# Optimization experiments

Hardware: AMD Instinct MI355X
Metric: run time of the kernel (lower is better)

Reference implementation:

```python
import jax, jax.numpy as jnp
import numpy as np

EPS = 1e-5

def _bn(h, g, b, m, v):
    # h: (B, Ch, L); BatchNorm1d in eval mode over channel axis 1
    inv = jax.lax.rsqrt(v + EPS)
    return (h - m[None, :, None]) * (inv * g)[None, :, None] + b[None, :, None]

def setup_inputs() -> dict:
    key = jax.random.key(0)
    ks = jax.random.split(key, 12)
    B, C, N = 32, 256, 4096
    N8, C8 = N // 8, C // 8
    x = jax.random.normal(ks[0], (B, C, N), dtype=jnp.float32)
    Wq = jax.random.normal(ks[1], (N8, N), dtype=jnp.float32) * (1.0 / np.sqrt(N))
    Wk = jax.random.normal(ks[2], (N8, N), dtype=jnp.float32) * (1.0 / np.sqrt(N))
    bn1_g = jnp.ones((N8,), jnp.float32); bn1_b = jnp.zeros((N8,), jnp.float32)
    bn1_m = jax.random.normal(ks[3], (N8,), jnp.float32) * 0.1
    bn1_v = jax.random.uniform(ks[4], (N8,), jnp.float32, 0.5, 1.5)
    bn2_g = jnp.ones((N8,), jnp.float32); bn2_b = jnp.zeros((N8,), jnp.float32)
    bn2_m = jax.random.normal(ks[5], (N8,), jnp.float32) * 0.1
    bn2_v = jax.random.uniform(ks[6], (N8,), jnp.float32, 0.5, 1.5)
    W1 = jax.random.normal(ks[7], (C8, C), dtype=jnp.float32) * (1.0 / np.sqrt(C))
    W2 = jax.random.normal(ks[8], (C, C8), dtype=jnp.float32) * (1.0 / np.sqrt(C8))
    alpha = jax.random.normal(ks[9], (1,), dtype=jnp.float32)
    return {"x": x, "Wq": Wq, "bn1_g": bn1_g, "bn1_b": bn1_b, "bn1_m": bn1_m, "bn1_v": bn1_v,
            "Wk": Wk, "bn2_g": bn2_g, "bn2_b": bn2_b, "bn2_m": bn2_m, "bn2_v": bn2_v,
            "W1": W1, "W2": W2, "alpha": alpha}

def reference(x, Wq, bn1_g, bn1_b, bn1_m, bn1_v, Wk, bn2_g, bn2_b, bn2_m, bn2_v, W1, W2, alpha):
    # x: (B, C, N); x_hat: (B, N, C) -- conv1d with kernel 1 == matmul over N axis
    x_hat = jnp.transpose(x, (0, 2, 1))
    q = jax.nn.relu(_bn(jnp.einsum('qn,bnc->bqc', Wq, x_hat), bn1_g, bn1_b, bn1_m, bn1_v))  # (B, N8, C)
    k = jax.nn.relu(_bn(jnp.einsum('qn,bnc->bqc', Wk, x_hat), bn2_g, bn2_b, bn2_m, bn2_v))  # (B, N8, C)
    sim = jnp.einsum('bkc,bkd->bcd', k, q)  # (B, C, C)
    aff = jax.nn.softmax(jnp.max(sim, axis=-1, keepdims=True) - sim, axis=-1)
    # squeeze-excite gating over channels
    pooled = jnp.max(x, axis=-1)  # (B, C) AdaptiveMaxPool1d(1)
    s = jax.nn.sigmoid(jax.nn.relu(pooled @ W1.T) @ W2.T)  # (B, C)
    gated = x * s[:, :, None]
    out = alpha[0] * jnp.einsum('bcd,bdn->bcn', aff, gated) + x
    return out
```

## Files before the change

### kernel.cpp

```cpp
#include <hip/hip_runtime.h>
#include <math.h>

#define B_   32
#define C_   256
#define N_   4096
#define N8_  512
#define C8_  32
#define EPS_ 1e-5f

typedef __attribute__((ext_vector_type(8))) short short8;
typedef __attribute__((ext_vector_type(4))) float f32x4;

__device__ __forceinline__ ushort f2bf(float v) {
  unsigned u = __float_as_uint(v);
  unsigned r = (u + 0x7fffu + ((u >> 16) & 1u)) >> 16;
  return (ushort)r;
}
__device__ __forceinline__ float bf2f(ushort h) {
  return __uint_as_float(((unsigned)h) << 16);
}

__global__ __launch_bounds__(256) void k_cvt(const float* __restrict__ src,
                                             ushort* __restrict__ hi,
                                             ushort* __restrict__ lo, int n4) {
  int i = blockIdx.x * 256 + threadIdx.x;
  int stride = gridDim.x * 256;
  for (; i < n4; i += stride) {
    float4 v = ((const float4*)src)[i];
    ushort4 h, l;
    h.x = f2bf(v.x); l.x = f2bf(v.x - bf2f(h.x));
    h.y = f2bf(v.y); l.y = f2bf(v.y - bf2f(h.y));
    h.z = f2bf(v.z); l.z = f2bf(v.z - bf2f(h.z));
    h.w = f2bf(v.w); l.w = f2bf(v.w - bf2f(h.w));
    ((ushort4*)hi)[i] = h;
    ((ushort4*)lo)[i] = l;
  }
}

__global__ __launch_bounds__(256) void k_cvt_x(const float* __restrict__ x,
    ushort* __restrict__ xh, ushort* __restrict__ xl,
    ushort* __restrict__ xTh, float* __restrict__ partial) {
  int b = blockIdx.z, cb = blockIdx.y, nb = blockIdx.x;
  int t = threadIdx.x;
  int cl  = t >> 2;
  int nl0 = (t & 3) * 16;
  const float* xp = x + ((size_t)b * C_ + cb * 64 + cl) * N_ + nb * 64 + nl0;
  float v[16];
  *(float4*)&v[0]  = *(const float4*)(xp + 0);
  *(float4*)&v[4]  = *(const float4*)(xp + 4);
  *(float4*)&v[8]  = *(const float4*)(xp + 8);
  *(float4*)&v[12] = *(const float4*)(xp + 12);
  ushort h[16], l[16];
  float mx = -3.402823466e+38f;
  #pragma unroll
  for (int j = 0; j < 16; ++j) {
    h[j] = f2bf(v[j]);
    l[j] = f2bf(v[j] - bf2f(h[j]));
    mx = fmaxf(mx, v[j]);
  }
  size_t fbase = ((size_t)b * C_ + cb * 64 + cl) * N_ + nb * 64 + nl0;
  *(short8*)(xh + fbase)     = *(short8*)&h[0];
  *(short8*)(xh + fbase + 8) = *(short8*)&h[8];
  *(short8*)(xl + fbase)     = *(short8*)&l[0];
  *(short8*)(xl + fbase + 8) = *(short8*)&l[8];
  mx = fmaxf(mx, __shfl_xor(mx, 1, 64));
  mx = fmaxf(mx, __shfl_xor(mx, 2, 64));
  if ((t & 3) == 0)
    partial[((size_t)b * C_ + cb * 64 + cl) * 64 + nb] = mx;
  __shared__ ushort lds[64 * 66];
  #pragma unroll
  for (int j = 0; j < 16; ++j) lds[cl * 66 + nl0 + j] = h[j];
  __syncthreads();
  int nr = t >> 2;
  int c0 = (t & 3) * 16;
  ushort o[16];
  #pragma unroll
  for (int j = 0; j < 16; ++j) o[j] = lds[(c0 + j) * 66 + nr];
  size_t tbase = ((size_t)b * N_ + nb * 64 + nr) * C_ + cb * 64 + c0;
  *(short8*)(xTh + tbase)     = *(short8*)&o[0];
  *(short8*)(xTh + tbase + 8) = *(short8*)&o[8];
}

__global__ __launch_bounds__(256) void k_semlp(const float* __restrict__ partial,
                                               const float* __restrict__ W1,
                                               const float* __restrict__ W2,
                                               float* __restrict__ s) {
  int b = blockIdx.x, t = threadIdx.x;
  __shared__ float p[C_];
  __shared__ float h[C8_];
  float m = -3.402823466e+38f;
  const float* pp = partial + ((size_t)b * C_ + t) * 64;
  #pragma unroll
  for (int j = 0; j < 64; ++j) m = fmaxf(m, pp[j]);
  p[t] = m;
  __syncthreads();
  if (t < C8_) {
    float a = 0.f;
    for (int c = 0; c < C_; ++c) a = fmaf(p[c], W1[t * C_ + c], a);
    h[t] = fmaxf(a, 0.f);
  }
  __syncthreads();
  float a = 0.f;
  #pragma unroll
  for (int j = 0; j < C8_; ++j) a = fmaf(h[j], W2[t * C8_ + j], a);
  s[b * C_ + t] = 1.f / (1.f + __expf(-a));
}

#define GLD16(SRC, DSTP) __builtin_amdgcn_global_load_lds( \
    (const __attribute__((address_space(1))) void*)(SRC), \
    (__attribute__((address_space(3))) void*)(DSTP), 16, 0, 0)

__global__ __launch_bounds__(512, 2) void k_qk8(
    const ushort* __restrict__ wh, const ushort* __restrict__ wl,
    const ushort* __restrict__ xh, const ushort* __restrict__ xl,
    float* __restrict__ part) {
  __shared__ ushort lds[2][2][256 * 64];
  const int bid = blockIdx.x;
  const int xcd = bid & 7, slot = bid >> 3;
  const int b   = xcd * 4 + (slot & 3);
  const int role = slot >> 2;
  const int ks = role & 1;
  const int mt = role >> 1;
  const int t = threadIdx.x;
  const int lane = t & 63, wave = t >> 6;
  const int wm = wave >> 2, wn = wave & 3;
  const int fr = lane & 15, quad = lane >> 4;
  const int R0 = mt * 256;
  const int tr = t >> 3, tc = (t & 7) << 3;
  int aro[4], bro[4];
#pragma unroll
  for (int j = 0; j < 4; ++j) {
    int rl = j * 64 + tr;
    int cu = tc ^ ((rl & 7) << 3);
    aro[j] = (R0 + rl) * N_ + cu;
    bro[j] = (b * C_ + rl) * N_ + cu;
  }
  const int dl = t * 8;

  f32x4 acc[8][4];
#pragma unroll
  for (int m = 0; m < 8; ++m)
#pragma unroll
    for (int n = 0; n < 4; ++n) acc[m][n] = (f32x4){0.f, 0.f, 0.f, 0.f};

  short8 af[4][2];
  short8 bf[2][2][2];

#define STG_A(AP, K0, P, J0) do { \
    GLD16((AP) + (aro[J0] + (K0)), &lds[P][0][(J0) * 4096 + dl]); \
    GLD16((AP) + (aro[(J0) + 1] + (K0)), &lds[P][0][((J0) + 1) * 4096 + dl]); \
  } while (0)
#define STG_B(BP, K0, P, J0) do { \
    GLD16((BP) + (bro[J0] + (K0)), &lds[P][1][(J0) * 4096 + dl]); \
    GLD16((BP) + (bro[(J0) + 1] + (K0)), &lds[P][1][((J0) + 1) * 4096 + dl]); \
  } while (0)
#define VMC(N) asm volatile("s_waitcnt vmcnt(" #N ")" ::: "memory")
#define BARF() do { __builtin_amdgcn_s_barrier(); \
                    __builtin_amdgcn_sched_barrier(0); } while (0)
#define RDA(P, MH) do { \
    _Pragma("unroll") \
    for (int m = 0; m < 4; ++m) { \
      int r = wm * 128 + ((MH) * 4 + m) * 16 + fr; \
      int o = (r << 6); \
      int sw = (r & 7) << 3; \
      af[m][0] = *(const short8*)&lds[P][0][o + ((quad << 3) ^ sw)]; \
      af[m][1] = *(const short8*)&lds[P][0][o + (((quad << 3) + 32) ^ sw)]; \
    } } while (0)
#define RDB(P, NH) do { \
    _Pragma("unroll") \
    for (int n = 0; n < 2; ++n) { \
      int c = wn * 64 + ((NH) * 2 + n) * 16 + fr; \
      int o = (c << 6); \
      int sw = (c & 7) << 3; \
      bf[NH][n][0] = *(const short8*)&lds[P][1][o + ((quad << 3) ^ sw)]; \
      bf[NH][n][1] = *(const short8*)&lds[P][1][o + (((quad << 3) + 32) ^ sw)]; \
    } } while (0)
#define MMQ(MH, NH) do { \
    __builtin_amdgcn_s_setprio(1); \
    _Pragma("unroll") \
    for (int m = 0; m < 4; ++m) \
      _Pragma("unroll") \
      for (int n = 0; n < 2; ++n) { \
        acc[(MH)*4+m][(NH)*2+n] = __builtin_amdgcn_mfma_f32_16x16x32_bf16( \
            af[m][0], bf[NH][n][0], acc[(MH)*4+m][(NH)*2+n], 0, 0, 0); \
        acc[(MH)*4+m][(NH)*2+n] = __builtin_amdgcn_mfma_f32_16x16x32_bf16( \
            af[m][1], bf[NH][n][1], acc[(MH)*4+m][(NH)*2+n], 0, 0, 0); \
      } \
    __builtin_amdgcn_s_setprio(0); } while (0)

  const int gbase = ks * 96;
  {
    int g = gbase, sg = g >> 6, k0 = (g & 63) << 6;
    const ushort* Ap = (sg == 1) ? wl : wh;
    const ushort* Bp = (sg == 2) ? xl : xh;
    STG_A(Ap, k0, 0, 0); STG_A(Ap, k0, 0, 2);
    STG_B(Bp, k0, 0, 0); STG_B(Bp, k0, 0, 2);
    int g1 = gbase + 1, s1 = g1 >> 6, k1 = (g1 & 63) << 6;
    const ushort* Ap1 = (s1 == 1) ? wl : wh;
    STG_A(Ap1, k1, 1, 0);
  }

#pragma unroll 1
  for (int i = 0; i < 48; ++i) {
    int gO = gbase + 2 * i + 1, sO = gO >> 6, kO = (gO & 63) << 6;
    const ushort* AO = (sO == 1) ? wl : wh;
    const ushort* BO = (sO == 2) ? xl : xh;
    int gE = gbase + 2 * i + 2, sE = gE >> 6, kE = (gE & 63) << 6;
    const ushort* AE = (sE == 1) ? wl : wh;
    const ushort* BE = (sE == 2) ? xl : xh;
    int gP = gbase + 2 * i + 3, sP = gP >> 6, kP = (gP & 63) << 6;
    const ushort* APn = (sP == 1) ? wl : wh;
    const bool nl = (i < 47);
    STG_A(AO, kO, 1, 2);
    VMC(4); BARF();
    RDA(0, 0); RDB(0, 0); MMQ(0, 0);
    STG_B(BO, kO, 1, 0);
    RDB(0, 1); MMQ(0, 1);
    STG_B(BO, kO, 1, 2);
    RDA(0, 1); MMQ(1, 0);
    BARF();
    if (nl) STG_A(AE, kE, 0, 0);
    MMQ(1, 1);
    if (nl) { STG_A(AE, kE, 0, 2); VMC(4); } else { VMC(0); }
    BARF();
    RDA(1, 0); RDB(1, 0); MMQ(0, 0);
    if (nl) STG_B(BE, kE, 0, 0);
    RDB(1, 1); MMQ(0, 1);
    if (nl) STG_B(BE, kE, 0, 2);
    RDA(1, 1); MMQ(1, 0);
    BARF();
    if (nl) STG_A(APn, kP, 1, 0);
    MMQ(1, 1);
  }

  float* dst = part + ((size_t)(ks * 32 + b) * 1024) * 256;
#pragma unroll
  for (int m = 0; m < 8; ++m) {
    int row0 = R0 + wm * 128 + m * 16 + quad * 4;
#pragma unroll
    for (int r = 0; r < 4; ++r) {
#pragma unroll
      for (int n = 0; n < 4; ++n) {
        int col = wn * 64 + n * 16 + fr;
        dst[(size_t)(row0 + r) * 256 + col] = acc[m][n][r];
      }
    }
  }
#undef STG_A
#undef STG_B
#undef VMC
#undef BARF
#undef RDA
#undef RDB
#undef MMQ
}

__global__ __launch_bounds__(256) void k_qkred(
    const float* __restrict__ part,
    const float* __restrict__ g1, const float* __restrict__ b1,
    const float* __restrict__ m1, const float* __restrict__ v1,
    const float* __restrict__ g2, const float* __restrict__ b2,
    const float* __restrict__ m2, const float* __restrict__ v2,
    float* __restrict__ q, float* __restrict__ k) {
  int i = blockIdx.x * 256 + threadIdx.x;
  int b = i >> 16;
  int rem = i & 65535;
  int row = rem >> 6;
  int c4 = (rem & 63) << 2;
  const float4* p = (const float4*)part;
  float4 u = p[i];
  float4 w = p[i + 2097152];
  bool isq = row < 512;
  int m = isq ? row : row - 512;
  float sc = (isq ? g1 : g2)[m] * rsqrtf((isq ? v1 : v2)[m] + EPS_);
  float bi = (isq ? b1 : b2)[m] - (isq ? m1 : m2)[m] * sc;
  float4 o;
  o.x = fmaxf(fmaf(u.x + w.x, sc, bi), 0.f);
  o.y = fmaxf(fmaf(u.y + w.y, sc, bi), 0.f);
  o.z = fmaxf(fmaf(u.z + w.z, sc, bi), 0.f);
  o.w = fmaxf(fmaf(u.w + w.w, sc, bi), 0.f);
  float* d = (isq ? q : k) + ((size_t)b * N8_ + m) * C_ + c4;
  *(float4*)d = o;
}

__global__ __launch_bounds__(256) void k_simsoft(const float* __restrict__ q,
    const float* __restrict__ k, const float* __restrict__ s,
    const float* __restrict__ alpha, ushort* __restrict__ aff2) {
  int b = blockIdx.y, ct = blockIdx.x;
  int t = threadIdx.x;
  __shared__ float kT[N8_][16];
  const float* kb = k + (size_t)b * N8_ * C_;
  int c0 = ct * 16;
  for (int chunk = 0; chunk < N8_ / 16; ++chunk) {
    int row = chunk * 16 + (t >> 4);
    kT[row][t & 15] = kb[(size_t)row * C_ + c0 + (t & 15)];
  }
  __syncthreads();
  float acc[16];
  #pragma unroll
  for (int i = 0; i < 16; ++i) acc[i] = 0.f;
  const float* qb = q + (size_t)b * N8_ * C_;
  for (int kk = 0; kk < N8_; ++kk) {
    float qv = qb[(size_t)kk * C_ + t];
    float4 k0 = *(const float4*)&kT[kk][0];
    float4 k1 = *(const float4*)&kT[kk][4];
    float4 k2 = *(const float4*)&kT[kk][8];
    float4 k3 = *(const float4*)&kT[kk][12];
    acc[0]  = fmaf(k0.x, qv, acc[0]);  acc[1]  = fmaf(k0.y, qv, acc[1]);
    acc[2]  = fmaf(k0.z, qv, acc[2]);  acc[3]  = fmaf(k0.w, qv, acc[3]);
    acc[4]  = fmaf(k1.x, qv, acc[4]);  acc[5]  = fmaf(k1.y, qv, acc[5]);
    acc[6]  = fmaf(k1.z, qv, acc[6]);  acc[7]  = fmaf(k1.w, qv, acc[7]);
    acc[8]  = fmaf(k2.x, qv, acc[8]);  acc[9]  = fmaf(k2.y, qv, acc[9]);
    acc[10] = fmaf(k2.z, qv, acc[10]); acc[11] = fmaf(k2.w, qv, acc[11]);
    acc[12] = fmaf(k3.x, qv, acc[12]); acc[13] = fmaf(k3.y, qv, acc[13]);
    acc[14] = fmaf(k3.z, qv, acc[14]); acc[15] = fmaf(k3.w, qv, acc[15]);
  }
  int lane = t & 63, wid = t >> 6;
  __shared__ float wmin[16][4];
  __shared__ float wsum[16][4];
  #pragma unroll
  for (int i = 0; i < 16; ++i) {
    float v = acc[i];
    for (int off = 32; off > 0; off >>= 1) v = fminf(v, __shfl_xor(v, off, 64));
    if (lane == 0) wmin[i][wid] = v;
  }
  __syncthreads();
  float w[16];
  #pragma unroll
  for (int i = 0; i < 16; ++i) {
    float m = fminf(fminf(wmin[i][0], wmin[i][1]), fminf(wmin[i][2], wmin[i][3]));
    w[i] = __expf(m - acc[i]);
  }
  #pragma unroll
  for (int i = 0; i < 16; ++i) {
    float v = w[i];
    for (int off = 32; off > 0; off >>= 1) v += __shfl_xor(v, off, 64);
    if (lane == 0) wsum[i][wid] = v;
  }
  __syncthreads();
  float fac = alpha[0] * s[b * C_ + t];
  ushort* ab = aff2 + (size_t)b * C_ * C_;
  #pragma unroll
  for (int i = 0; i < 16; ++i) {
    float Z = wsum[i][0] + wsum[i][1] + wsum[i][2] + wsum[i][3];
    ab[(size_t)(c0 + i) * C_ + t] = f2bf(fac * w[i] / Z);
  }
}

__global__ __launch_bounds__(256) void k_out_mfma(
    const ushort* __restrict__ aff, const ushort* __restrict__ xTh,
    const float* __restrict__ x, float* __restrict__ out) {
  int b  = blockIdx.z;
  int cb = blockIdx.y;
  int nb = blockIdx.x;
  __shared__ ushort Ah[128 * 32];
  __shared__ ushort Bh[128 * 32];
  int t = threadIdx.x, wave = t >> 6, lane = t & 63;
  int wr = (wave >> 1) * 64, wc = (wave & 1) * 64;
  int srow = wave * 16 + (lane >> 2);
  int skof = (lane & 3) * 8;
  size_t aoff = ((size_t)b * C_ + cb * 128 + srow) * C_ + skof;
  size_t boff = ((size_t)b * N_ + nb * 128 + srow) * C_ + skof;
  int lb0 = (wave * 16) * 32;

  f32x4 acc[4][4];
  #pragma unroll
  for (int mi = 0; mi < 4; ++mi)
    #pragma unroll
    for (int ni = 0; ni < 4; ++ni)
      acc[mi][ni] = (f32x4){0.f, 0.f, 0.f, 0.f};

  int fr = lane & 15, quad = lane >> 4;
  for (int k0 = 0; k0 < C_; k0 += 32) {
    #pragma unroll
    for (int seg = 0; seg < 2; ++seg) {
      size_t ga = aoff + (size_t)seg * 64 * C_ + k0;
      size_t gb = boff + (size_t)seg * 64 * C_ + k0;
      int lb = lb0 + seg * 64 * 32;
      __builtin_amdgcn_global_load_lds(
          (const __attribute__((address_space(1))) void*)(aff + ga),
          (__attribute__((address_space(3))) void*)(&Ah[lb]), 16, 0, 0);
      __builtin_amdgcn_global_load_lds(
          (const __attribute__((address_space(1))) void*)(xTh + gb),
          (__attribute__((address_space(3))) void*)(&Bh[lb]), 16, 0, 0);
    }
    __syncthreads();
    short8 af[4], bf[4];
    #pragma unroll
    for (int i = 0; i < 4; ++i) {
      af[i] = *(const short8*)&Ah[(wr + i * 16 + fr) * 32 + quad * 8];
      bf[i] = *(const short8*)&Bh[(wc + i * 16 + fr) * 32 + quad * 8];
    }
    #pragma unroll
    for (int mi = 0; mi < 4; ++mi)
      #pragma unroll
      for (int ni = 0; ni < 4; ++ni)
        acc[mi][ni] = __builtin_amdgcn_mfma_f32_16x16x32_bf16(
            af[mi], bf[ni], acc[mi][ni], 0, 0, 0);
    __syncthreads();
  }

  const float* xb = x + (size_t)b * C_ * N_;
  float* ob = out + (size_t)b * C_ * N_;
  int c0 = cb * 128 + wr + quad * 4;
  int n0 = nb * 128 + wc + fr;
  #pragma unroll
  for (int mi = 0; mi < 4; ++mi) {
    #pragma unroll
    for (int r = 0; r < 4; ++r) {
      int c = c0 + mi * 16 + r;
      #pragma unroll
      for (int ni = 0; ni < 4; ++ni) {
        int n = n0 + ni * 16;
        ob[(size_t)c * N_ + n] = acc[mi][ni][r] + xb[(size_t)c * N_ + n];
      }
    }
  }
}

extern "C" void kernel_launch(void* const* d_in, const int* in_sizes, int n_in,
                              void* d_out, int out_size, void* d_ws, size_t ws_size,
                              hipStream_t stream) {
  const float* x     = (const float*)d_in[0];
  const float* Wq    = (const float*)d_in[1];
  const float* g1    = (const float*)d_in[2];
  const float* b1    = (const float*)d_in[3];
  const float* m1    = (const float*)d_in[4];
  const float* v1    = (const float*)d_in[5];
  const float* Wk    = (const float*)d_in[6];
  const float* g2    = (const float*)d_in[7];
  const float* b2    = (const float*)d_in[8];
  const float* m2    = (const float*)d_in[9];
  const float* v2    = (const float*)d_in[10];
  const float* W1    = (const float*)d_in[11];
  const float* W2    = (const float*)d_in[12];
  const float* alpha = (const float*)d_in[13];
  float* out = (float*)d_out;

  float* ws      = (float*)d_ws;
  float* q       = ws;
  float* kbuf    = q + (size_t)B_ * N8_ * C_;
  float* partial = kbuf + (size_t)B_ * N8_ * C_;
  float* s       = partial + (size_t)B_ * C_ * 64;
  ushort* aff    = (ushort*)(s + B_ * C_);
  ushort* xh     = aff + (size_t)B_ * C_ * C_;
  ushort* xl     = xh + (size_t)B_ * C_ * N_;
  ushort* xTh    = xl + (size_t)B_ * C_ * N_;
  ushort* wh     = xTh + (size_t)B_ * C_ * N_;
  ushort* wl     = wh + (size_t)2 * N8_ * N_;

  float* gpart = (float*)d_out;

  k_cvt_x<<<dim3(64, 4, B_), 256, 0, stream>>>(x, xh, xl, xTh, partial);
  k_cvt<<<dim3(1024), 256, 0, stream>>>(Wq, wh, wl, N8_ * N_ / 4);
  k_cvt<<<dim3(1024), 256, 0, stream>>>(Wk, wh + (size_t)N8_ * N_,
                                        wl + (size_t)N8_ * N_, N8_ * N_ / 4);
  k_semlp<<<dim3(B_), 256, 0, stream>>>(partial, W1, W2, s);
  k_qk8<<<dim3(256), 512, 0, stream>>>(wh, wl, xh, xl, gpart);
  k_qkred<<<dim3(8192), 256, 0, stream>>>(gpart, g1, b1, m1, v1,
                                          g2, b2, m2, v2, q, kbuf);
  k_simsoft<<<dim3(16, B_), 256, 0, stream>>>(q, kbuf, s, alpha, aff);
  k_out_mfma<<<dim3(32, 2, B_), 256, 0, stream>>>(aff, xTh, x, out);
}
```

Before: 648.9 us.

## Restructure QK GEMM main loop to double-buffer LDS fragments row-by-row

Rewrites the software pipeline of the split-K bf16 MFMA GEMM. Instead of staging A and B in halves interleaved with quadrant MFMA groups, each stage now issues all global-to-LDS loads at once after a barrier. LDS fragment reads are ping-ponged one A row at a time against MFMAs, and the next buffer's first fragments are prefetched before the last MFMAs finish. The aim is to hide LDS read latency and cut the number of barriers per tile, at the cost of a more complex prologue and epilogue and a different vmcnt wait discipline.

```diff
diff --git a/kernel.cpp b/kernel.cpp
--- a/kernel.cpp
+++ b/kernel.cpp
@@ -143,95 +143,107 @@
 #pragma unroll
     for (int n = 0; n < 4; ++n) acc[m][n] = (f32x4){0.f, 0.f, 0.f, 0.f};
 
-  short8 af[4][2];
-  short8 bf[2][2][2];
-
-#define STG_A(AP, K0, P, J0) do { \
-    GLD16((AP) + (aro[J0] + (K0)), &lds[P][0][(J0) * 4096 + dl]); \
-    GLD16((AP) + (aro[(J0) + 1] + (K0)), &lds[P][0][((J0) + 1) * 4096 + dl]); \
+  short8 afA_[2], afB_[2];
+  short8 b0[2][2], b1[2][2];
+
+#define STG(AP, BP, K0, P) do { \
+    GLD16((AP) + (aro[0] + (K0)), &lds[P][0][0 * 4096 + dl]); \
+    GLD16((AP) + (aro[1] + (K0)), &lds[P][0][1 * 4096 + dl]); \
+    GLD16((AP) + (aro[2] + (K0)), &lds[P][0][2 * 4096 + dl]); \
+    GLD16((AP) + (aro[3] + (K0)), &lds[P][0][3 * 4096 + dl]); \
+    GLD16((BP) + (bro[0] + (K0)), &lds[P][1][0 * 4096 + dl]); \
+    GLD16((BP) + (bro[1] + (K0)), &lds[P][1][1 * 4096 + dl]); \
+    GLD16((BP) + (bro[2] + (K0)), &lds[P][1][2 * 4096 + dl]); \
+    GLD16((BP) + (bro[3] + (K0)), &lds[P][1][3 * 4096 + dl]); \
   } while (0)
-#define STG_B(BP, K0, P, J0) do { \
-    GLD16((BP) + (bro[J0] + (K0)), &lds[P][1][(J0) * 4096 + dl]); \
-    GLD16((BP) + (bro[(J0) + 1] + (K0)), &lds[P][1][((J0) + 1) * 4096 + dl]); \
-  } while (0)
-#define VMC(N) asm volatile("s_waitcnt vmcnt(" #N ")" ::: "memory")
+#define VMC8 asm volatile("s_waitcnt vmcnt(8)" ::: "memory")
+#define VMC0 asm volatile("s_waitcnt vmcnt(0)" ::: "memory")
+#define LGKM0 asm volatile("s_waitcnt lgkmcnt(0)" ::: "memory")
 #define BARF() do { __builtin_amdgcn_s_barrier(); \
                     __builtin_amdgcn_sched_barrier(0); } while (0)
-#define RDA(P, MH) do { \
-    _Pragma("unroll") \
-    for (int m = 0; m < 4; ++m) { \
-      int r = wm * 128 + ((MH) * 4 + m) * 16 + fr; \
-      int o = (r << 6); \
-      int sw = (r & 7) << 3; \
-      af[m][0] = *(const short8*)&lds[P][0][o + ((quad << 3) ^ sw)]; \
-      af[m][1] = *(const short8*)&lds[P][0][o + (((quad << 3) + 32) ^ sw)]; \
-    } } while (0)
-#define RDB(P, NH) do { \
+#define MFMA_(A, Bb, Cc) __builtin_amdgcn_mfma_f32_16x16x32_bf16(A, Bb, Cc, 0, 0, 0)
+#define RDROW(P, DST, RIDX) do { \
+    int rr_ = wm * 128 + (RIDX) * 16 + fr; \
+    int o_ = (rr_ << 6); int sw_ = (rr_ & 7) << 3; \
+    DST[0] = *(const short8*)&lds[P][0][o_ + ((quad << 3) ^ sw_)]; \
+    DST[1] = *(const short8*)&lds[P][0][o_ + (((quad << 3) + 32) ^ sw_)]; \
+  } while (0)
+#define RDBX(P, BF, NH) do { \
     _Pragma("unroll") \
     for (int n = 0; n < 2; ++n) { \
-      int c = wn * 64 + ((NH) * 2 + n) * 16 + fr; \
-      int o = (c << 6); \
-      int sw = (c & 7) << 3; \
-      bf[NH][n][0] = *(const short8*)&lds[P][1][o + ((quad << 3) ^ sw)]; \
-      bf[NH][n][1] = *(const short8*)&lds[P][1][o + (((quad << 3) + 32) ^ sw)]; \
+      int c_ = wn * 64 + ((NH) * 2 + n) * 16 + fr; \
+      int o_ = (c_ << 6); int sw_ = (c_ & 7) << 3; \
+      BF[n][0] = *(const short8*)&lds[P][1][o_ + ((quad << 3) ^ sw_)]; \
+      BF[n][1] = *(const short8*)&lds[P][1][o_ + (((quad << 3) + 32) ^ sw_)]; \
     } } while (0)
-#define MMQ(MH, NH) do { \
+#define MM8(S, AF) do { \
     __builtin_amdgcn_s_setprio(1); \
-    _Pragma("unroll") \
-    for (int m = 0; m < 4; ++m) \
-      _Pragma("unroll") \
-      for (int n = 0; n < 2; ++n) { \
-        acc[(MH)*4+m][(NH)*2+n] = __builtin_amdgcn_mfma_f32_16x16x32_bf16( \
-            af[m][0], bf[NH][n][0], acc[(MH)*4+m][(NH)*2+n], 0, 0, 0); \
-        acc[(MH)*4+m][(NH)*2+n] = __builtin_amdgcn_mfma_f32_16x16x32_bf16( \
-            af[m][1], bf[NH][n][1], acc[(MH)*4+m][(NH)*2+n], 0, 0, 0); \
-      } \
+    acc[S][0] = MFMA_(AF[0], b0[0][0], acc[S][0]); \
+    acc[S][0] = MFMA_(AF[1], b0[0][1], acc[S][0]); \
+    acc[S][1] = MFMA_(AF[0], b0[1][0], acc[S][1]); \
+    acc[S][1] = MFMA_(AF[1], b0[1][1], acc[S][1]); \
+    acc[S][2] = MFMA_(AF[0], b1[0][0], acc[S][2]); \
+    acc[S][2] = MFMA_(AF[1], b1[0][1], acc[S][2]); \
+    acc[S][3] = MFMA_(AF[0], b1[1][0], acc[S][3]); \
+    acc[S][3] = MFMA_(AF[1], b1[1][1], acc[S][3]); \
     __builtin_amdgcn_s_setprio(0); } while (0)
+#define MM4(S, AF, BF, CB) do { \
+    __builtin_amdgcn_s_setprio(1); \
+    acc[S][(CB) + 0] = MFMA_(AF[0], BF[0][0], acc[S][(CB) + 0]); \
+    acc[S][(CB) + 0] = MFMA_(AF[1], BF[0][1], acc[S][(CB) + 0]); \
+    acc[S][(CB) + 1] = MFMA_(AF[0], BF[1][0], acc[S][(CB) + 1]); \
+    acc[S][(CB) + 1] = MFMA_(AF[1], BF[1][1], acc[S][(CB) + 1]); \
+    __builtin_amdgcn_s_setprio(0); } while (0)
+#define BLOCK(P, PN, APs, BPs, KS, DOSTG, VMCST, DORD) do { \
+    RDROW(P, afB_, 1); MM8(0, afA_); \
+    RDROW(P, afA_, 2); MM8(1, afB_); \
+    RDROW(P, afB_, 3); MM8(2, afA_); \
+    RDROW(P, afA_, 4); MM8(3, afB_); \
+    RDROW(P, afB_, 5); MM8(4, afA_); \
+    RDROW(P, afA_, 6); MM8(5, afB_); \
+    RDROW(P, afB_, 7); MM8(6, afA_); \
+    LGKM0; \
+    BARF(); \
+    if (DOSTG) STG(APs, BPs, KS, P); \
+    VMCST; \
+    BARF(); \
+    if (DORD) RDROW(PN, afA_, 0); \
+    MM4(7, afB_, b0, 0); \
+    if (DORD) RDBX(PN, b0, 0); \
+    MM4(7, afB_, b1, 2); \
+    if (DORD) RDBX(PN, b1, 1); \
+  } while (0)
 
   const int gbase = ks * 96;
   {
-    int g = gbase, sg = g >> 6, k0 = (g & 63) << 6;
-    const ushort* Ap = (sg == 1) ? wl : wh;
-    const ushort* Bp = (sg == 2) ? xl : xh;
-    STG_A(Ap, k0, 0, 0); STG_A(Ap, k0, 0, 2);
-    STG_B(Bp, k0, 0, 0); STG_B(Bp, k0, 0, 2);
-    int g1 = gbase + 1, s1 = g1 >> 6, k1 = (g1 & 63) << 6;
-    const ushort* Ap1 = (s1 == 1) ? wl : wh;
-    STG_A(Ap1, k1, 1, 0);
-  }
+    int g0 = gbase, s0 = g0 >> 6, k0p = (g0 & 63) << 6;
+    const ushort* A0 = (s0 == 1) ? wl : wh;
+    const ushort* B0 = (s0 == 2) ? xl : xh;
+    STG(A0, B0, k0p, 0);
+    int g1 = gbase + 1, s1 = g1 >> 6, k1p = (g1 & 63) << 6;
+    const ushort* A1 = (s1 == 1) ? wl : wh;
+    const ushort* B1 = (s1 == 2) ? xl : xh;
+    STG(A1, B1, k1p, 1);
+  }
+  VMC8;
+  BARF();
+  RDROW(0, afA_, 0);
+  RDBX(0, b0, 0);
+  RDBX(0, b1, 1);
 
 #pragma unroll 1
-  for (int i = 0; i < 48; ++i) {
-    int gO = gbase + 2 * i + 1, sO = gO >> 6, kO = (gO & 63) << 6;
-    const ushort* AO = (sO == 1) ? wl : wh;
-    const ushort* BO = (sO == 2) ? xl : xh;
-    int gE = gbase + 2 * i + 2, sE = gE >> 6, kE = (gE & 63) << 6;
-    const ushort* AE = (sE == 1) ? wl : wh;
-    const ushort* BE = (sE == 2) ? xl : xh;
-    int gP = gbase + 2 * i + 3, sP = gP >> 6, kP = (gP & 63) << 6;
-    const ushort* APn = (sP == 1) ? wl : wh;
-    const bool nl = (i < 47);
-    STG_A(AO, kO, 1, 2);
-    VMC(4); BARF();
-    RDA(0, 0); RDB(0, 0); MMQ(0, 0);
-    STG_B(BO, kO, 1, 0);
-    RDB(0, 1); MMQ(0, 1);
-    STG_B(BO, kO, 1, 2);
-    RDA(0, 1); MMQ(1, 0);
-    BARF();
-    if (nl) STG_A(AE, kE, 0, 0);
-    MMQ(1, 1);
-    if (nl) { STG_A(AE, kE, 0, 2); VMC(4); } else { VMC(0); }
-    BARF();
-    RDA(1, 0); RDB(1, 0); MMQ(0, 0);
-    if (nl) STG_B(BE, kE, 0, 0);
-    RDB(1, 1); MMQ(0, 1);
-    if (nl) STG_B(BE, kE, 0, 2);
-    RDA(1, 1); MMQ(1, 0);
-    BARF();
-    if (nl) STG_A(APn, kP, 1, 0);
-    MMQ(1, 1);
-  }
+  for (int i = 0; i < 47; ++i) {
+    int g2 = gbase + 2 * i + 2, s2 = g2 >> 6, k2 = (g2 & 63) << 6;
+    const ushort* A2 = (s2 == 1) ? wl : wh;
+    const ushort* B2 = (s2 == 2) ? xl : xh;
+    int g3 = gbase + 2 * i + 3, s3 = g3 >> 6, k3 = (g3 & 63) << 6;
+    const ushort* A3 = (s3 == 1) ? wl : wh;
+    const ushort* B3 = (s3 == 2) ? xl : xh;
+    BLOCK(0, 1, A2, B2, k2, 1, VMC8, 1);
+    BLOCK(1, 0, A3, B3, k3, 1, VMC8, 1);
+  }
+  BLOCK(0, 1, wh, xh, 0, 0, VMC0, 1);
+  BLOCK(1, 0, wh, xh, 0, 0, VMC0, 0);
 
   float* dst = part + ((size_t)(ks * 32 + b) * 1024) * 256;
 #pragma unroll
@@ -246,13 +258,17 @@
       }
     }
   }
-#undef STG_A
-#undef STG_B
-#undef VMC
+#undef STG
+#undef VMC8
+#undef VMC0
+#undef LGKM0
 #undef BARF
-#undef RDA
-#undef RDB
-#undef MMQ
+#undef MFMA_
+#undef RDROW
+#undef RDBX
+#undef MM8
+#undef MM4
+#undef BLOCK
 }
 
 __global__ __launch_bounds__(256) void k_qkred(
```

Measured after the change: 645.4 us. About the same (-0.5%).

## Restructure QK GEMM main loop into four-phase ping-pong tile schedule

Applied to the files above, without the earlier changes.

Rewrites the bf16 MFMA main loop of the QK projection GEMM. Each K-tile is now processed in four sub-phases: B fragments are loaded once per tile, A fragments two rows at a time, and global-to-LDS staging of the next tile is spread across the phases. Explicit barriers and lgkmcnt waits separate LDS reads from MFMA bursts. This replaces the previous partially staggered prefetch schedule, which used vmcnt(4) waits, with full vmcnt(0) waits per tile and many more barriers. The aim is a cleaner overlap of loads and matrix math with fewer live fragment registers, at the cost of more synchronisation.

```diff
diff --git a/kernel.cpp b/kernel.cpp
--- a/kernel.cpp
+++ b/kernel.cpp
@@ -143,8 +143,8 @@
 #pragma unroll
     for (int n = 0; n < 4; ++n) acc[m][n] = (f32x4){0.f, 0.f, 0.f, 0.f};
 
-  short8 af[4][2];
-  short8 bf[2][2][2];
+  short8 af[2][2];
+  short8 bb[4][2];
 
 #define STG_A(AP, K0, P, J0) do { \
     GLD16((AP) + (aro[J0] + (K0)), &lds[P][0][(J0) * 4096 + dl]); \
@@ -154,83 +154,69 @@
     GLD16((BP) + (bro[J0] + (K0)), &lds[P][1][(J0) * 4096 + dl]); \
     GLD16((BP) + (bro[(J0) + 1] + (K0)), &lds[P][1][((J0) + 1) * 4096 + dl]); \
   } while (0)
-#define VMC(N) asm volatile("s_waitcnt vmcnt(" #N ")" ::: "memory")
-#define BARF() do { __builtin_amdgcn_s_barrier(); \
-                    __builtin_amdgcn_sched_barrier(0); } while (0)
-#define RDA(P, MH) do { \
+#define VMC0 asm volatile("s_waitcnt vmcnt(0)" ::: "memory")
+#define LGKM0 asm volatile("s_waitcnt lgkmcnt(0)" ::: "memory")
+#define SB0 __builtin_amdgcn_sched_barrier(0)
+#define BARF() do { __builtin_amdgcn_s_barrier(); SB0; } while (0)
+#define MFMA_(A, Bb, Cc) __builtin_amdgcn_mfma_f32_16x16x32_bf16(A, Bb, Cc, 0, 0, 0)
+#define RDA2(P, MP) do { \
     _Pragma("unroll") \
-    for (int m = 0; m < 4; ++m) { \
-      int r = wm * 128 + ((MH) * 4 + m) * 16 + fr; \
-      int o = (r << 6); \
-      int sw = (r & 7) << 3; \
-      af[m][0] = *(const short8*)&lds[P][0][o + ((quad << 3) ^ sw)]; \
-      af[m][1] = *(const short8*)&lds[P][0][o + (((quad << 3) + 32) ^ sw)]; \
+    for (int j = 0; j < 2; ++j) { \
+      int r_ = wm * 128 + ((MP) * 2 + j) * 16 + fr; \
+      int o_ = (r_ << 6); int sw_ = (r_ & 7) << 3; \
+      af[j][0] = *(const short8*)&lds[P][0][o_ + ((quad << 3) ^ sw_)]; \
+      af[j][1] = *(const short8*)&lds[P][0][o_ + (((quad << 3) + 32) ^ sw_)]; \
     } } while (0)
-#define RDB(P, NH) do { \
+#define RDB4(P) do { \
     _Pragma("unroll") \
-    for (int n = 0; n < 2; ++n) { \
-      int c = wn * 64 + ((NH) * 2 + n) * 16 + fr; \
-      int o = (c << 6); \
-      int sw = (c & 7) << 3; \
-      bf[NH][n][0] = *(const short8*)&lds[P][1][o + ((quad << 3) ^ sw)]; \
-      bf[NH][n][1] = *(const short8*)&lds[P][1][o + (((quad << 3) + 32) ^ sw)]; \
+    for (int n = 0; n < 4; ++n) { \
+      int c_ = wn * 64 + n * 16 + fr; \
+      int o_ = (c_ << 6); int sw_ = (c_ & 7) << 3; \
+      bb[n][0] = *(const short8*)&lds[P][1][o_ + ((quad << 3) ^ sw_)]; \
+      bb[n][1] = *(const short8*)&lds[P][1][o_ + (((quad << 3) + 32) ^ sw_)]; \
     } } while (0)
-#define MMQ(MH, NH) do { \
+#define MMP(MP) do { \
     __builtin_amdgcn_s_setprio(1); \
     _Pragma("unroll") \
-    for (int m = 0; m < 4; ++m) \
+    for (int j = 0; j < 2; ++j) \
       _Pragma("unroll") \
-      for (int n = 0; n < 2; ++n) { \
-        acc[(MH)*4+m][(NH)*2+n] = __builtin_amdgcn_mfma_f32_16x16x32_bf16( \
-            af[m][0], bf[NH][n][0], acc[(MH)*4+m][(NH)*2+n], 0, 0, 0); \
-        acc[(MH)*4+m][(NH)*2+n] = __builtin_amdgcn_mfma_f32_16x16x32_bf16( \
-            af[m][1], bf[NH][n][1], acc[(MH)*4+m][(NH)*2+n], 0, 0, 0); \
+      for (int n = 0; n < 4; ++n) { \
+        acc[(MP)*2+j][n] = MFMA_(af[j][0], bb[n][0], acc[(MP)*2+j][n]); \
+        acc[(MP)*2+j][n] = MFMA_(af[j][1], bb[n][1], acc[(MP)*2+j][n]); \
       } \
     __builtin_amdgcn_s_setprio(0); } while (0)
+#define TILE(P, PN, GN, DOSTG) do { \
+    int sn_ = (GN) >> 6, kn_ = ((GN) & 63) << 6; \
+    const ushort* An_ = (sn_ == 1) ? wl : wh; \
+    const ushort* Bn_ = (sn_ == 2) ? xl : xh; \
+    VMC0; BARF(); \
+    RDB4(P); RDA2(P, 0); \
+    if (DOSTG) { STG_A(An_, kn_, PN, 0); STG_A(An_, kn_, PN, 2); } \
+    BARF(); LGKM0; SB0; MMP(0); BARF(); \
+    RDA2(P, 1); \
+    if (DOSTG) STG_B(Bn_, kn_, PN, 0); \
+    BARF(); LGKM0; SB0; MMP(1); BARF(); \
+    RDA2(P, 2); \
+    if (DOSTG) STG_B(Bn_, kn_, PN, 2); \
+    BARF(); LGKM0; SB0; MMP(2); BARF(); \
+    RDA2(P, 3); \
+    BARF(); LGKM0; SB0; MMP(3); \
+  } while (0)
 
   const int gbase = ks * 96;
   {
-    int g = gbase, sg = g >> 6, k0 = (g & 63) << 6;
-    const ushort* Ap = (sg == 1) ? wl : wh;
-    const ushort* Bp = (sg == 2) ? xl : xh;
-    STG_A(Ap, k0, 0, 0); STG_A(Ap, k0, 0, 2);
-    STG_B(Bp, k0, 0, 0); STG_B(Bp, k0, 0, 2);
-    int g1 = gbase + 1, s1 = g1 >> 6, k1 = (g1 & 63) << 6;
-    const ushort* Ap1 = (s1 == 1) ? wl : wh;
-    STG_A(Ap1, k1, 1, 0);
+    int g0 = gbase, s0 = g0 >> 6, k0p = (g0 & 63) << 6;
+    const ushort* A0 = (s0 == 1) ? wl : wh;
+    const ushort* B0 = (s0 == 2) ? xl : xh;
+    STG_A(A0, k0p, 0, 0); STG_A(A0, k0p, 0, 2);
+    STG_B(B0, k0p, 0, 0); STG_B(B0, k0p, 0, 2);
   }
 
 #pragma unroll 1
   for (int i = 0; i < 48; ++i) {
-    int gO = gbase + 2 * i + 1, sO = gO >> 6, kO = (gO & 63) << 6;
-    const ushort* AO = (sO == 1) ? wl : wh;
-    const ushort* BO = (sO == 2) ? xl : xh;
-    int gE = gbase + 2 * i + 2, sE = gE >> 6, kE = (gE & 63) << 6;
-    const ushort* AE = (sE == 1) ? wl : wh;
-    const ushort* BE = (sE == 2) ? xl : xh;
-    int gP = gbase + 2 * i + 3, sP = gP >> 6, kP = (gP & 63) << 6;
-    const ushort* APn = (sP == 1) ? wl : wh;
-    const bool nl = (i < 47);
-    STG_A(AO, kO, 1, 2);
-    VMC(4); BARF();
-    RDA(0, 0); RDB(0, 0); MMQ(0, 0);
-    STG_B(BO, kO, 1, 0);
-    RDB(0, 1); MMQ(0, 1);
-    STG_B(BO, kO, 1, 2);
-    RDA(0, 1); MMQ(1, 0);
-    BARF();
-    if (nl) STG_A(AE, kE, 0, 0);
-    MMQ(1, 1);
-    if (nl) { STG_A(AE, kE, 0, 2); VMC(4); } else { VMC(0); }
-    BARF();
-    RDA(1, 0); RDB(1, 0); MMQ(0, 0);
-    if (nl) STG_B(BE, kE, 0, 0);
-    RDB(1, 1); MMQ(0, 1);
-    if (nl) STG_B(BE, kE, 0, 2);
-    RDA(1, 1); MMQ(1, 0);
-    BARF();
-    if (nl) STG_A(APn, kP, 1, 0);
-    MMQ(1, 1);
+    int t0 = gbase + 2 * i;
+    TILE(0, 1, t0 + 1, 1);
+    TILE(1, 0, t0 + 2, (i < 47));
   }
 
   float* dst = part + ((size_t)(ks * 32 + b) * 1024) * 256;
@@ -248,11 +234,15 @@
   }
 #undef STG_A
 #undef STG_B
-#undef VMC
+#undef VMC0
+#undef LGKM0
+#undef SB0
 #undef BARF
-#undef RDA
-#undef RDB
-#undef MMQ
+#undef MFMA_
+#undef RDA2
+#undef RDB4
+#undef MMP
+#undef TILE
 }
 
 __global__ __launch_bounds__(256) void k_qkred(
```

Measured after the change: 665.2 us. 1.03x slower.
